# Kernel optimization log

Hardware: AMD Instinct MI355X
Metric: run time of the kernel (lower is better)

The kernel has to match this reference:

```python
import jax, jax.numpy as jnp
import numpy as np

B, LQ, LKV, C, H, Z = 4, 1024, 4096, 256, 8, 1024


def setup_inputs() -> dict:
    key = jax.random.key(0)
    ks = jax.random.split(key, 10)
    s = 0.02  # small init scale for weights
    return {
        "q": jax.random.normal(ks[0], (B, LQ, C), jnp.float32),
        "kv": jax.random.normal(ks[1], (B, LKV, C), jnp.float32),
        "q_ape": jax.random.normal(ks[2], (1, LQ, C), jnp.float32),
        "k_ape": jax.random.normal(ks[3], (1, LKV - Z, C), jnp.float32),
        "attn_pos": jax.random.normal(ks[4], (1, H, LQ, Z), jnp.float32),
        "Wq": jax.random.normal(ks[5], (C, C), jnp.float32) * s,
        "Wk": jax.random.normal(ks[6], (C, C), jnp.float32) * s,
        "Wv": jax.random.normal(ks[7], (C, C), jnp.float32) * s,
        "Wp": jax.random.normal(ks[8], (C, C), jnp.float32) * s,
        "bp": jnp.zeros((C,), jnp.float32),
        "z_shape": Z,
    }


def reference(q, kv, q_ape, k_ape, attn_pos, Wq, Wk, Wv, Wp, bp, z_shape):
    Bn, Lq, Cd = q.shape
    d = Cd // H
    scale = d ** (-0.5)
    # q path: APE added before projection
    qh = ((q + q_ape) @ Wq.T).reshape(Bn, Lq, H, d).transpose(0, 2, 1, 3)  # (B,H,Lq,d)
    # in-place `k[:, z_shape:, :] += k_ape` in torch aliases kv, so v also sees it
    kvm = kv.at[:, z_shape:, :].add(k_ape)
    kh = (kvm @ Wk.T).reshape(Bn, -1, H, d).transpose(0, 2, 1, 3)  # (B,H,Lkv,d)
    vh = (kvm @ Wv.T).reshape(Bn, -1, H, d).transpose(0, 2, 1, 3)  # (B,H,Lkv,d)
    attn = jnp.einsum('bhqd,bhkd->bhqk', qh, kh) * scale           # (B,H,Lq,Lkv)
    # partial positional bias on the template slice only
    attn = attn.at[:, :, :, :z_shape].add(attn_pos)
    attn = jax.nn.softmax(attn, axis=-1)
    x = jnp.einsum('bhqk,bhkd->bhqd', attn, vh)
    x = x.transpose(0, 2, 1, 3).reshape(Bn, Lq, Cd)
    return x @ Wp.T + bp
```

## Files before the change

kernel.cpp:

```cpp
#include <hip/hip_runtime.h>


typedef __attribute__((ext_vector_type(8))) short bf16x8;
typedef __attribute__((ext_vector_type(4))) float f32x4;
typedef __attribute__((ext_vector_type(4))) unsigned short u16x4;

#define MFMA16(a, b, c) __builtin_amdgcn_mfma_f32_16x16x32_bf16((a), (b), (c), 0, 0, 0)

__device__ __forceinline__ unsigned short f2bf(float f) {
  return __builtin_bit_cast(unsigned short, static_cast<__bf16>(f));
}
__device__ __forceinline__ float bf2f(unsigned short u) {
  return __builtin_bit_cast(float, ((unsigned)u) << 16);
}

__global__ __launch_bounds__(256) void prep_all(const float* __restrict__ Wq,
                                                const float* __restrict__ Wk,
                                                const float* __restrict__ Wv,
                                                const float* __restrict__ Wp,
                                                const float* __restrict__ pos,
                                                const float* __restrict__ Xq,
                                                const float* __restrict__ Xkv,
                                                const float* __restrict__ q_ape,
                                                const float* __restrict__ k_ape,
                                                unsigned short* __restrict__ wout,
                                                unsigned short* __restrict__ pfb,
                                                unsigned short* __restrict__ kvp,
                                                unsigned short* __restrict__ qp,
                                                int posBlocks) {
  int bx = blockIdx.x;
  if (bx < posBlocks) {
    const int s4 = bx * 256 + threadIdx.x;
    const int zk4 = s4 & 255, q = (s4 >> 8) & 1023, h = s4 >> 18;
    const float4 v = *(const float4*)(pos + ((size_t)s4 << 2));
    const int kt = zk4 >> 4, c = (zk4 >> 2) & 3, g = zk4 & 3;
    const float L = 1.4426950408889634f;
    u16x4 o = { f2bf(v.x * L), f2bf(v.y * L), f2bf(v.z * L), f2bf(v.w * L) };
    *(u16x4*)(pfb + (size_t)((h << 6) + (q >> 4)) * 16384 + ((kt << 2) + c) * 256 + ((q & 15) << 4) + (g << 2)) = o;
    return;
  }
  bx -= posBlocks;
  if (bx < 128) {
    const int idx = bx * 256 + threadIdx.x;
    const int which = idx >> 13, rem = idx & 8191;
    const int o = rem >> 5, colb = (rem & 31) << 3;
    const float* src = (which == 0) ? Wq : (which == 1) ? Wk : (which == 2) ? Wv : Wp;
    float4 v0 = *(const float4*)(src + (size_t)o * 256 + colb);
    float4 v1 = *(const float4*)(src + (size_t)o * 256 + colb + 4);
    if (which == 0) {
      const float qs = 0.17677669529663687f * 1.4426950408889634f;
      v0.x *= qs; v0.y *= qs; v0.z *= qs; v0.w *= qs;
      v1.x *= qs; v1.y *= qs; v1.z *= qs; v1.w *= qs;
    }
    const int n = o >> 4, x = o & 15, k = colb >> 5, g = (colb & 31) >> 3;
    unsigned short* dst = wout + (which << 16) + n * 4096 + k * 512 + x * 32 + g * 8;
    u16x4 a = { f2bf(v0.x), f2bf(v0.y), f2bf(v0.z), f2bf(v0.w) };
    u16x4 b = { f2bf(v1.x), f2bf(v1.y), f2bf(v1.z), f2bf(v1.w) };
    *(u16x4*)dst = a;
    *(u16x4*)(dst + 4) = b;
    return;
  }
  bx -= 128;
  if (bx < 2048) {
    const int idx = bx * 256 + threadIdx.x;
    const int row = idx >> 5, c8 = idx & 31;
    const int col = c8 << 3, lq = row & 4095;
    const float* xp = Xkv + (size_t)row * 256 + col;
    float4 v0 = *(const float4*)xp, v1 = *(const float4*)(xp + 4);
    if (lq >= 1024) {
      const float* ap = k_ape + (size_t)(lq - 1024) * 256 + col;
      const float4 a0 = *(const float4*)ap, a1 = *(const float4*)(ap + 4);
      v0.x += a0.x; v0.y += a0.y; v0.z += a0.z; v0.w += a0.w;
      v1.x += a1.x; v1.y += a1.y; v1.z += a1.z; v1.w += a1.w;
    }
    const int k = c8 >> 2, g = c8 & 3;
    unsigned short* dst = kvp + (size_t)(row >> 4) * 4096 + k * 512 + (row & 15) * 32 + g * 8;
    u16x4 a = { f2bf(v0.x), f2bf(v0.y), f2bf(v0.z), f2bf(v0.w) };
    u16x4 b = { f2bf(v1.x), f2bf(v1.y), f2bf(v1.z), f2bf(v1.w) };
    *(u16x4*)dst = a;
    *(u16x4*)(dst + 4) = b;
    return;
  }
  bx -= 2048;
  {
    const int idx = bx * 256 + threadIdx.x;
    const int row = idx >> 5, c8 = idx & 31;
    const int col = c8 << 3, arow = row & 1023;
    const float* xp = Xq + (size_t)row * 256 + col;
    const float* ap = q_ape + (size_t)arow * 256 + col;
    const float4 v0 = *(const float4*)xp, v1 = *(const float4*)(xp + 4);
    const float4 a0 = *(const float4*)ap, a1 = *(const float4*)(ap + 4);
    const int k = c8 >> 2, g = c8 & 3;
    unsigned short* dst = qp + (size_t)(row >> 4) * 4096 + k * 512 + (row & 15) * 32 + g * 8;
    u16x4 a = { f2bf(v0.x + a0.x), f2bf(v0.y + a0.y), f2bf(v0.z + a0.z), f2bf(v0.w + a0.w) };
    u16x4 b = { f2bf(v1.x + a1.x), f2bf(v1.y + a1.y), f2bf(v1.z + a1.z), f2bf(v1.w + a1.w) };
    *(u16x4*)dst = a;
    *(u16x4*)(dst + 4) = b;
  }
}

__global__ __launch_bounds__(256, 4) void proj_qkv(const unsigned short* __restrict__ kvp,
                                                   const unsigned short* __restrict__ qp,
                                                   const unsigned short* __restrict__ Wqb,
                                                   const unsigned short* __restrict__ Wkb,
                                                   const unsigned short* __restrict__ Wvb,
                                                   unsigned short* __restrict__ Qhp,
                                                   unsigned short* __restrict__ Khp,
                                                   unsigned short* __restrict__ Vsp) {
  const int tid = threadIdx.x;
  const int w = tid >> 6, lane = tid & 63, x = lane & 15, g = lane >> 4;
  const int rg = w & 1, nh = w >> 1;
  const int bx = blockIdx.x;
  if (bx < 1024) {
    const bool isV = bx >= 512;
    const int bk = isV ? bx - 512 : bx;
    const int rbase = bk * 32 + rg * 16;
    const unsigned short* ap = kvp + (size_t)(rbase >> 4) * 4096 + x * 32 + g * 8;
    bf16x8 a[8];
#pragma unroll
    for (int k = 0; k < 8; ++k) a[k] = *(const bf16x8*)(ap + k * 512);
    const unsigned short* Wb = isV ? Wvb : Wkb;
    f32x4 acc[8];
#pragma unroll
    for (int n = 0; n < 8; ++n) acc[n] = (f32x4){0.f, 0.f, 0.f, 0.f};
#pragma unroll
    for (int k = 0; k < 8; ++k)
#pragma unroll
      for (int n0 = 0; n0 < 8; ++n0) {
        const bf16x8 bw = *(const bf16x8*)(Wb + (size_t)(nh * 8 + n0) * 4096 + k * 512 + x * 32 + g * 8);
        acc[n0] = MFMA16(a[k], bw, acc[n0]);
      }
    if (!isV) {
      const int b2 = rbase >> 12, kk0 = (rbase & 4095) + g * 4;
#pragma unroll
      for (int n0 = 0; n0 < 8; ++n0) {
        const int n = nh * 8 + n0, hh = n >> 1, dd = ((n & 1) << 4) + x;
        unsigned short* kp = Khp + (size_t)(b2 * 8 + hh) * 131072;
#pragma unroll
        for (int r = 0; r < 4; ++r)
          kp[(size_t)(kk0 + r) * 32 + dd] = f2bf(acc[n0][r]);
      }
    } else {
      const int b2 = rbase >> 12, T = (rbase >> 6) & 63, c0 = (rbase >> 4) & 3;
      const int ks = c0 & 1, ih = (c0 >> 1) << 2;
#pragma unroll
      for (int n0 = 0; n0 < 8; ++n0) {
        const int n = nh * 8 + n0, hh = n >> 1, dh = n & 1;
        u16x4 o = { f2bf(acc[n0][0]), f2bf(acc[n0][1]), f2bf(acc[n0][2]), f2bf(acc[n0][3]) };
        *(u16x4*)(Vsp + (size_t)(b2 * 8 + hh) * 131072 + T * 2048 + ks * 1024 + dh * 512 + g * 128 + x * 8 + ih) = o;
      }
    }
  } else {
    const int bq = bx - 1024;
    const int rbase = bq * 32 + rg * 16;
    const unsigned short* ap = qp + (size_t)(rbase >> 4) * 4096 + x * 32 + g * 8;
    bf16x8 a[8];
#pragma unroll
    for (int k = 0; k < 8; ++k) a[k] = *(const bf16x8*)(ap + k * 512);
    f32x4 acc[8];
#pragma unroll
    for (int n = 0; n < 8; ++n) acc[n] = (f32x4){0.f, 0.f, 0.f, 0.f};
#pragma unroll
    for (int k = 0; k < 8; ++k)
#pragma unroll
      for (int n0 = 0; n0 < 8; ++n0) {
        const bf16x8 bw = *(const bf16x8*)(Wqb + (size_t)(nh * 8 + n0) * 4096 + k * 512 + x * 32 + g * 8);
        acc[n0] = MFMA16(a[k], bw, acc[n0]);
      }
    const int b2 = rbase >> 10, qr0 = (rbase & 1023) + g * 4;
#pragma unroll
    for (int n0 = 0; n0 < 8; ++n0) {
      const int n = nh * 8 + n0, hh = n >> 1, dd = ((n & 1) << 4) + x;
      unsigned short* qpn = Qhp + (size_t)(b2 * 8 + hh) * 32768;
#pragma unroll
      for (int r = 0; r < 4; ++r)
        qpn[(size_t)(qr0 + r) * 32 + dd] = f2bf(acc[n0][r]);
    }
  }
}

template <int SPLIT, bool PF>
__global__ __launch_bounds__(256, 4) void
attn_fused(const unsigned short* __restrict__ Qhp,
           const unsigned short* __restrict__ Khp,
           const unsigned short* __restrict__ Vsp,
           const void* __restrict__ pos,
           unsigned short* __restrict__ Xo,
           float* __restrict__ Opart,
           float* __restrict__ lpart) {
  const int tid = threadIdx.x;
  const int w = tid >> 6, lane = tid & 63, x = lane & 15, g = lane >> 4;
  const int bid = blockIdx.x;
  const int h = bid & 7, b = (bid >> 3) & 3, qt = (bid >> 5) & 7, z = bid >> 8;
  const int qrow0 = qt * 128 + w * 32;
  const int NT = 64 / SPLIT;

  const unsigned short* Qpl = Qhp + (size_t)(b * 8 + h) * 32768;
  const bf16x8 aq0 = *(const bf16x8*)(Qpl + (size_t)(qrow0 + x) * 32 + g * 8);
  const bf16x8 aq1 = *(const bf16x8*)(Qpl + (size_t)(qrow0 + 16 + x) * 32 + g * 8);
  const unsigned short* Kpl = Khp + (size_t)(b * 8 + h) * 131072 + x * 32 + g * 8;
  const unsigned short* Vpl = Vsp + (size_t)(b * 8 + h) * 131072 + g * 128 + x * 8;
  const unsigned short* pq0 = PF ? (const unsigned short*)pos + (size_t)((h << 6) + (qt << 3) + (w << 1)) * 16384 : nullptr;
  const unsigned short* pq1 = PF ? pq0 + 16384 : nullptr;
  const float* pr0 = PF ? nullptr : (const float*)pos + (size_t)((h << 10) + qrow0 + x) * 1024;
  const float* pr1 = PF ? nullptr : (const float*)pos + (size_t)((h << 10) + qrow0 + 16 + x) * 1024;
  const f32x4 zc = {0.f, 0.f, 0.f, 0.f};

  f32x4 o00 = zc, o01 = zc, o10 = zc, o11 = zc;
  float ls0 = 0.f, ls1 = 0.f;

  bf16x8 ka[4], va[4];
#pragma unroll
  for (int c = 0; c < 4; ++c)
    ka[c] = *(const bf16x8*)(Kpl + (size_t)((z << 6) + c * 16) * 32);
#pragma unroll
  for (int j = 0; j < 4; ++j)
    va[j] = *(const bf16x8*)(Vpl + (z << 11) + (j << 9));

#define GROUP(AQ, PQ, PR, LS, OA, OB, T, BIAS)                                               \
  do {                                                                                       \
    f32x4 s[4];                                                                              \
    _Pragma("unroll")                                                                        \
    for (int c = 0; c < 4; ++c) s[c] = MFMA16(ka[c], AQ, zc);                                \
    if (BIAS) {                                                                              \
      if (PF) {                                                                              \
        _Pragma("unroll")                                                                    \
        for (int c = 0; c < 4; ++c) {                                                        \
          const u16x4 p = *(const u16x4*)(PQ + ((T) << 10) + (c << 8) + (x << 4) + (g << 2)); \
          s[c][0] += bf2f(p[0]); s[c][1] += bf2f(p[1]);                                      \
          s[c][2] += bf2f(p[2]); s[c][3] += bf2f(p[3]);                                      \
        }                                                                                    \
      } else {                                                                               \
        const float LOG2E = 1.4426950408889634f;                                             \
        _Pragma("unroll")                                                                    \
        for (int c = 0; c < 4; ++c) {                                                        \
          const float4 p = *(const float4*)(PR + ((T) << 6) + c * 16 + g * 4);               \
          s[c][0] = fmaf(p.x, LOG2E, s[c][0]); s[c][1] = fmaf(p.y, LOG2E, s[c][1]);          \
          s[c][2] = fmaf(p.z, LOG2E, s[c][2]); s[c][3] = fmaf(p.w, LOG2E, s[c][3]);          \
        }                                                                                    \
      }                                                                                      \
    }                                                                                        \
    _Pragma("unroll")                                                                        \
    for (int c = 0; c < 4; ++c)                                                              \
      _Pragma("unroll")                                                                      \
      for (int r = 0; r < 4; ++r) {                                                          \
        s[c][r] = __builtin_amdgcn_exp2f(s[c][r]); LS += s[c][r];                            \
      }                                                                                      \
    bf16x8 pa0, pa1;                                                                         \
    _Pragma("unroll")                                                                        \
    for (int r = 0; r < 4; ++r) {                                                            \
      pa0[r] = (short)f2bf(s[0][r]); pa0[4 + r] = (short)f2bf(s[2][r]);                      \
      pa1[r] = (short)f2bf(s[1][r]); pa1[4 + r] = (short)f2bf(s[3][r]);                      \
    }                                                                                        \
    OA = MFMA16(pa0, va[0], OA); OB = MFMA16(pa0, va[1], OB);                                \
    OA = MFMA16(pa1, va[2], OA); OB = MFMA16(pa1, va[3], OB);                                \
  } while (0)

#define TILE(T, BIAS)                                                                        \
  do {                                                                                       \
    const int tp = ((T) + SPLIT <= 63) ? (T) + SPLIT : (T);                                  \
    GROUP(aq0, pq0, pr0, ls0, o00, o01, T, BIAS);                                            \
    GROUP(aq1, pq1, pr1, ls1, o10, o11, T, BIAS);                                            \
    _Pragma("unroll")                                                                        \
    for (int c = 0; c < 4; ++c)                            \
      ka[c] = *(const bf16x8*)(Kpl + (size_t)((tp << 6) + c * 16) * 32);                     \
    _Pragma("unroll")                                                                        \
    for (int j = 0; j < 4; ++j)                            \
      va[j] = *(const bf16x8*)(Vpl + (tp << 11) + (j << 9));                                 \
  } while (0)

  const int nb = 16 / SPLIT;
  int t = z;
  for (int i = 0; i < nb; ++i) { TILE(t, true);  t += SPLIT; }
  for (int i = nb; i < NT; ++i) { TILE(t, false); t += SPLIT; }
#undef TILE
#undef GROUP

  ls0 += __shfl_xor(ls0, 16); ls0 += __shfl_xor(ls0, 32);
  ls1 += __shfl_xor(ls1, 16); ls1 += __shfl_xor(ls1, 32);

  if (SPLIT == 1) {
    const float inv0 = 1.f / ls0, inv1 = 1.f / ls1;
#pragma unroll
    for (int r = 0; r < 4; ++r) {
      const float ir0 = __shfl(inv0, g * 4 + r, 64);
      const float ir1 = __shfl(inv1, g * 4 + r, 64);
      const size_t orow0 = (size_t)((b << 10) + qrow0 + g * 4 + r) * 256 + h * 32;
      const size_t orow1 = (size_t)((b << 10) + qrow0 + 16 + g * 4 + r) * 256 + h * 32;
      Xo[orow0 + x] = f2bf(o00[r] * ir0);
      Xo[orow0 + 16 + x] = f2bf(o01[r] * ir0);
      Xo[orow1 + x] = f2bf(o10[r] * ir1);
      Xo[orow1 + 16 + x] = f2bf(o11[r] * ir1);
    }
  } else {
    if (g == 0) {
      lpart[(size_t)z * 32768 + ((b << 10) + qrow0 + x) * 8 + h] = ls0;
      lpart[(size_t)z * 32768 + ((b << 10) + qrow0 + 16 + x) * 8 + h] = ls1;
    }
#pragma unroll
    for (int r = 0; r < 4; ++r) {
      const size_t orow0 = (size_t)z * 1048576 + (size_t)((b << 10) + qrow0 + g * 4 + r) * 256 + h * 32;
      const size_t orow1 = (size_t)z * 1048576 + (size_t)((b << 10) + qrow0 + 16 + g * 4 + r) * 256 + h * 32;
      Opart[orow0 + x] = o00[r];
      Opart[orow0 + 16 + x] = o01[r];
      Opart[orow1 + x] = o10[r];
      Opart[orow1 + 16 + x] = o11[r];
    }
  }
}

__global__ __launch_bounds__(256) void combine(const float* __restrict__ Opart,
                                               const float* __restrict__ lpart,
                                               unsigned short* __restrict__ Xo, int split) {
  const int idx = blockIdx.x * 256 + threadIdx.x;
  const int row = idx >> 6, c4 = (idx & 63) << 2, h = c4 >> 5;
  float l = 0.f;
  float4 o = {0.f, 0.f, 0.f, 0.f};
  for (int zz = 0; zz < split; ++zz) {
    l += lpart[(size_t)zz * 32768 + row * 8 + h];
    const float4 ov = *(const float4*)(Opart + (size_t)zz * 1048576 + (size_t)row * 256 + c4);
    o.x += ov.x; o.y += ov.y; o.z += ov.z; o.w += ov.w;
  }
  const float inv = 1.f / l;
  u16x4 pk = { f2bf(o.x * inv), f2bf(o.y * inv), f2bf(o.z * inv), f2bf(o.w * inv) };
  *(u16x4*)(Xo + (size_t)row * 256 + c4) = pk;
}

__global__ __launch_bounds__(256) void proj_out(const unsigned short* __restrict__ Xb,
                                                const unsigned short* __restrict__ Wb,
                                                const float* __restrict__ bias,
                                                float* __restrict__ out) {
  const int tid = threadIdx.x;
  const int w = tid >> 6, lane = tid & 63, x = lane & 15, g = lane >> 4;
  const int rbase = blockIdx.x << 4;
  const int cb = w << 6;
  bf16x8 a[8];
#pragma unroll
  for (int k = 0; k < 8; ++k)
    a[k] = *(const bf16x8*)(Xb + (size_t)(rbase + x) * 256 + k * 32 + g * 8);
  f32x4 acc[4];
#pragma unroll
  for (int n = 0; n < 4; ++n) acc[n] = (f32x4){0.f, 0.f, 0.f, 0.f};
#pragma unroll
  for (int k = 0; k < 8; ++k)
#pragma unroll
    for (int n = 0; n < 4; ++n) {
      const bf16x8 bw = *(const bf16x8*)(Wb + (size_t)((w << 2) + n) * 4096 + k * 512 + x * 32 + g * 8);
      acc[n] = MFMA16(a[k], bw, acc[n]);
    }
#pragma unroll
  for (int n = 0; n < 4; ++n) {
    const float bv = bias[cb + n * 16 + x];
#pragma unroll
    for (int r = 0; r < 4; ++r)
      out[(size_t)(rbase + g * 4 + r) * 256 + cb + n * 16 + x] = acc[n][r] + bv;
  }
}

extern "C" void kernel_launch(void* const* d_in, const int* in_sizes, int n_in,
                              void* d_out, int out_size, void* d_ws, size_t ws_size,
                              hipStream_t stream) {
  const float* q        = (const float*)d_in[0];
  const float* kv       = (const float*)d_in[1];
  const float* q_ape    = (const float*)d_in[2];
  const float* k_ape    = (const float*)d_in[3];
  const float* attn_pos = (const float*)d_in[4];
  const float* Wq       = (const float*)d_in[5];
  const float* Wk       = (const float*)d_in[6];
  const float* Wv       = (const float*)d_in[7];
  const float* Wp       = (const float*)d_in[8];
  const float* bp       = (const float*)d_in[9];
  float* out = (float*)d_out;

  unsigned short* wsb = (unsigned short*)d_ws;
  unsigned short* Wqb = wsb;
  unsigned short* Wkb = wsb + 65536;
  unsigned short* Wvb = wsb + 131072;
  unsigned short* Wpb = wsb + 196608;
  unsigned short* Qhp = wsb + 262144;
  unsigned short* Khp = wsb + 1310720;
  unsigned short* Vsp = wsb + 5505024;
  unsigned short* Xws = wsb + 9699328;
  unsigned short* kvp = wsb + 10747904;
  unsigned short* qp  = wsb + 14942208;

  const size_t L0  = 31981568ull;
  const size_t PFB = 16777216ull;
  const size_t PS  = 4325376ull;
  int split; bool havepf;
  if      (ws_size >= L0 + PFB + 4 * PS) { split = 4; havepf = true; }
  else if (ws_size >= L0 + 4 * PS)       { split = 4; havepf = false; }
  else if (ws_size >= L0 + 2 * PS)       { split = 2; havepf = false; }
  else                                   { split = 1; havepf = false; }
  unsigned short* pfb = (unsigned short*)((char*)d_ws + L0);
  float* Opart = (float*)((char*)d_ws + L0 + (havepf ? PFB : 0));
  float* lpart = Opart + (size_t)split * 1048576;

  const int posBlocks = havepf ? 8192 : 0;
  prep_all<<<posBlocks + 128 + 2048 + 512, 256, 0, stream>>>(
      Wq, Wk, Wv, Wp, attn_pos, q, kv, q_ape, k_ape, wsb, pfb, kvp, qp, posBlocks);
  proj_qkv<<<1152, 256, 0, stream>>>(kvp, qp, Wqb, Wkb, Wvb, Qhp, Khp, Vsp);
  if (havepf)
    attn_fused<4, true><<<1024, 256, 0, stream>>>(Qhp, Khp, Vsp, pfb, Xws, Opart, lpart);
  else if (split == 4)
    attn_fused<4, false><<<1024, 256, 0, stream>>>(Qhp, Khp, Vsp, attn_pos, Xws, Opart, lpart);
  else if (split == 2)
    attn_fused<2, false><<<512, 256, 0, stream>>>(Qhp, Khp, Vsp, attn_pos, Xws, Opart, lpart);
  else
    attn_fused<1, false><<<256, 256, 0, stream>>>(Qhp, Khp, Vsp, attn_pos, Xws, Opart, lpart);
  if (split > 1) combine<<<1024, 256, 0, stream>>>(Opart, lpart, Xws, split);
  proj_out<<<256, 256, 0, stream>>>(Xws, Wpb, bp, out);
}
```

Baseline: 88.84 us.

## Process 64 query rows per wave, raise KV split to 8, pre-tile attention output

Each wave now handles four 16-row query groups instead of two, so every K/V fragment loaded from global memory is reused across twice as many query rows. To keep the grid size, the KV dimension is split eight ways when workspace allows. The combine and single-split paths now write the attention output in an MFMA-fragment tiled layout, which proj_out reads contiguously. The cost is more accumulator registers per wave, which may lower occupancy under the 4-blocks launch bound, plus more partial outputs for combine to read and sum.

```diff
diff --git a/kernel.cpp b/kernel.cpp
--- a/kernel.cpp
+++ b/kernel.cpp
@@ -191,23 +191,25 @@
   const int tid = threadIdx.x;
   const int w = tid >> 6, lane = tid & 63, x = lane & 15, g = lane >> 4;
   const int bid = blockIdx.x;
-  const int h = bid & 7, b = (bid >> 3) & 3, qt = (bid >> 5) & 7, z = bid >> 8;
-  const int qrow0 = qt * 128 + w * 32;
+  const int h = bid & 7, b = (bid >> 3) & 3, qt = (bid >> 5) & 3, z = bid >> 7;
+  const int qrow0 = qt * 256 + w * 64;
   const int NT = 64 / SPLIT;
 
   const unsigned short* Qpl = Qhp + (size_t)(b * 8 + h) * 32768;
-  const bf16x8 aq0 = *(const bf16x8*)(Qpl + (size_t)(qrow0 + x) * 32 + g * 8);
-  const bf16x8 aq1 = *(const bf16x8*)(Qpl + (size_t)(qrow0 + 16 + x) * 32 + g * 8);
+  bf16x8 aq[4];
+#pragma unroll
+  for (int gi = 0; gi < 4; ++gi)
+    aq[gi] = *(const bf16x8*)(Qpl + (size_t)(qrow0 + gi * 16 + x) * 32 + g * 8);
   const unsigned short* Kpl = Khp + (size_t)(b * 8 + h) * 131072 + x * 32 + g * 8;
   const unsigned short* Vpl = Vsp + (size_t)(b * 8 + h) * 131072 + g * 128 + x * 8;
-  const unsigned short* pq0 = PF ? (const unsigned short*)pos + (size_t)((h << 6) + (qt << 3) + (w << 1)) * 16384 : nullptr;
-  const unsigned short* pq1 = PF ? pq0 + 16384 : nullptr;
-  const float* pr0 = PF ? nullptr : (const float*)pos + (size_t)((h << 10) + qrow0 + x) * 1024;
-  const float* pr1 = PF ? nullptr : (const float*)pos + (size_t)((h << 10) + qrow0 + 16 + x) * 1024;
+  const unsigned short* pqb = PF ? (const unsigned short*)pos + (size_t)((h << 6) + (qt << 4) + (w << 2)) * 16384 : nullptr;
+  const float* prb = PF ? nullptr : (const float*)pos + (size_t)((h << 10) + qrow0 + x) * 1024;
   const f32x4 zc = {0.f, 0.f, 0.f, 0.f};
 
-  f32x4 o00 = zc, o01 = zc, o10 = zc, o11 = zc;
-  float ls0 = 0.f, ls1 = 0.f;
+  f32x4 oA[4], oB[4];
+  float ls[4];
+#pragma unroll
+  for (int gi = 0; gi < 4; ++gi) { oA[gi] = zc; oB[gi] = zc; ls[gi] = 0.f; }
 
   bf16x8 ka[4], va[4];
 #pragma unroll
@@ -217,50 +219,53 @@
   for (int j = 0; j < 4; ++j)
     va[j] = *(const bf16x8*)(Vpl + (z << 11) + (j << 9));
 
-#define GROUP(AQ, PQ, PR, LS, OA, OB, T, BIAS)                                               \
+#define CPAIR(GI, C0, C1, V0, V1, T, BIAS)                                                   \
   do {                                                                                       \
-    f32x4 s[4];                                                                              \
-    _Pragma("unroll")                                                                        \
-    for (int c = 0; c < 4; ++c) s[c] = MFMA16(ka[c], AQ, zc);                                \
+    f32x4 s0 = MFMA16(ka[C0], aq[GI], zc);                                                   \
+    f32x4 s1 = MFMA16(ka[C1], aq[GI], zc);                                                   \
     if (BIAS) {                                                                              \
       if (PF) {                                                                              \
-        _Pragma("unroll")                                                                    \
-        for (int c = 0; c < 4; ++c) {                                                        \
-          const u16x4 p = *(const u16x4*)(PQ + ((T) << 10) + (c << 8) + (x << 4) + (g << 2)); \
-          s[c][0] += bf2f(p[0]); s[c][1] += bf2f(p[1]);                                      \
-          s[c][2] += bf2f(p[2]); s[c][3] += bf2f(p[3]);                                      \
-        }                                                                                    \
+        const unsigned short* pq = pqb + (size_t)(GI) * 16384;                               \
+        const u16x4 p0 = *(const u16x4*)(pq + ((T) << 10) + ((C0) << 8) + (x << 4) + (g << 2)); \
+        const u16x4 p1 = *(const u16x4*)(pq + ((T) << 10) + ((C1) << 8) + (x << 4) + (g << 2)); \
+        s0[0] += bf2f(p0[0]); s0[1] += bf2f(p0[1]); s0[2] += bf2f(p0[2]); s0[3] += bf2f(p0[3]); \
+        s1[0] += bf2f(p1[0]); s1[1] += bf2f(p1[1]); s1[2] += bf2f(p1[2]); s1[3] += bf2f(p1[3]); \
       } else {                                                                               \
         const float LOG2E = 1.4426950408889634f;                                             \
-        _Pragma("unroll")                                                                    \
-        for (int c = 0; c < 4; ++c) {                                                        \
-          const float4 p = *(const float4*)(PR + ((T) << 6) + c * 16 + g * 4);               \
-          s[c][0] = fmaf(p.x, LOG2E, s[c][0]); s[c][1] = fmaf(p.y, LOG2E, s[c][1]);          \
-          s[c][2] = fmaf(p.z, LOG2E, s[c][2]); s[c][3] = fmaf(p.w, LOG2E, s[c][3]);          \
-        }                                                                                    \
+        const float* pr = prb + (size_t)(GI) * 16384;                                        \
+        const float4 p0 = *(const float4*)(pr + ((T) << 6) + (C0) * 16 + g * 4);             \
+        const float4 p1 = *(const float4*)(pr + ((T) << 6) + (C1) * 16 + g * 4);             \
+        s0[0] = fmaf(p0.x, LOG2E, s0[0]); s0[1] = fmaf(p0.y, LOG2E, s0[1]);                  \
+        s0[2] = fmaf(p0.z, LOG2E, s0[2]); s0[3] = fmaf(p0.w, LOG2E, s0[3]);                  \
+        s1[0] = fmaf(p1.x, LOG2E, s1[0]); s1[1] = fmaf(p1.y, LOG2E, s1[1]);                  \
+        s1[2] = fmaf(p1.z, LOG2E, s1[2]); s1[3] = fmaf(p1.w, LOG2E, s1[3]);                  \
       }                                                                                      \
     }                                                                                        \
-    _Pragma("unroll")                                                                        \
-    for (int c = 0; c < 4; ++c)                                                              \
-      _Pragma("unroll")                                                                      \
-      for (int r = 0; r < 4; ++r) {                                                          \
-        s[c][r] = __builtin_amdgcn_exp2f(s[c][r]); LS += s[c][r];                            \
-      }                                                                                      \
-    bf16x8 pa0, pa1;                                                                         \
+    bf16x8 pa;                                                                               \
     _Pragma("unroll")                                                                        \
     for (int r = 0; r < 4; ++r) {                                                            \
-      pa0[r] = (short)f2bf(s[0][r]); pa0[4 + r] = (short)f2bf(s[2][r]);                      \
-      pa1[r] = (short)f2bf(s[1][r]); pa1[4 + r] = (short)f2bf(s[3][r]);                      \
+      s0[r] = __builtin_amdgcn_exp2f(s0[r]); ls[GI] += s0[r];                                \
+      s1[r] = __builtin_amdgcn_exp2f(s1[r]); ls[GI] += s1[r];                                \
+      pa[r] = (short)f2bf(s0[r]);                                                            \
+      pa[4 + r] = (short)f2bf(s1[r]);                                                        \
     }                                                                                        \
-    OA = MFMA16(pa0, va[0], OA); OB = MFMA16(pa0, va[1], OB);                                \
-    OA = MFMA16(pa1, va[2], OA); OB = MFMA16(pa1, va[3], OB);                                \
+    oA[GI] = MFMA16(pa, va[V0], oA[GI]);                                                     \
+    oB[GI] = MFMA16(pa, va[V1], oB[GI]);                                                     \
+  } while (0)
+
+#define GROUP(GI, T, BIAS)                                                                   \
+  do {                                                                                       \
+    CPAIR(GI, 0, 2, 0, 1, T, BIAS);                                                          \
+    CPAIR(GI, 1, 3, 2, 3, T, BIAS);                                                          \
   } while (0)
 
 #define TILE(T, BIAS)                                                                        \
   do {                                                                                       \
     const int tp = ((T) + SPLIT <= 63) ? (T) + SPLIT : (T);                                  \
-    GROUP(aq0, pq0, pr0, ls0, o00, o01, T, BIAS);                                            \
-    GROUP(aq1, pq1, pr1, ls1, o10, o11, T, BIAS);                                            \
+    GROUP(0, T, BIAS);                                                                       \
+    GROUP(1, T, BIAS);                                                                       \
+    GROUP(2, T, BIAS);                                                                       \
+    GROUP(3, T, BIAS);                                                                       \
     _Pragma("unroll")                                                                        \
     for (int c = 0; c < 4; ++c)                            \
       ka[c] = *(const bf16x8*)(Kpl + (size_t)((tp << 6) + c * 16) * 32);                     \
@@ -275,36 +280,39 @@
   for (int i = nb; i < NT; ++i) { TILE(t, false); t += SPLIT; }
 #undef TILE
 #undef GROUP
-
-  ls0 += __shfl_xor(ls0, 16); ls0 += __shfl_xor(ls0, 32);
-  ls1 += __shfl_xor(ls1, 16); ls1 += __shfl_xor(ls1, 32);
+#undef CPAIR
+
+#pragma unroll
+  for (int gi = 0; gi < 4; ++gi) {
+    ls[gi] += __shfl_xor(ls[gi], 16);
+    ls[gi] += __shfl_xor(ls[gi], 32);
+  }
 
   if (SPLIT == 1) {
-    const float inv0 = 1.f / ls0, inv1 = 1.f / ls1;
-#pragma unroll
-    for (int r = 0; r < 4; ++r) {
-      const float ir0 = __shfl(inv0, g * 4 + r, 64);
-      const float ir1 = __shfl(inv1, g * 4 + r, 64);
-      const size_t orow0 = (size_t)((b << 10) + qrow0 + g * 4 + r) * 256 + h * 32;
-      const size_t orow1 = (size_t)((b << 10) + qrow0 + 16 + g * 4 + r) * 256 + h * 32;
-      Xo[orow0 + x] = f2bf(o00[r] * ir0);
-      Xo[orow0 + 16 + x] = f2bf(o01[r] * ir0);
-      Xo[orow1 + x] = f2bf(o10[r] * ir1);
-      Xo[orow1 + 16 + x] = f2bf(o11[r] * ir1);
+#pragma unroll
+    for (int gi = 0; gi < 4; ++gi) {
+      const float inv = 1.f / ls[gi];
+      const int rowblk = (b << 6) + (qt << 4) + (w << 2) + gi;
+#pragma unroll
+      for (int r = 0; r < 4; ++r) {
+        const float ir = __shfl(inv, g * 4 + r, 64);
+        unsigned short* dst = Xo + (size_t)rowblk * 4096 + h * 512 + (g * 4 + r) * 32;
+        dst[x] = f2bf(oA[gi][r] * ir);
+        dst[16 + x] = f2bf(oB[gi][r] * ir);
+      }
     }
   } else {
-    if (g == 0) {
-      lpart[(size_t)z * 32768 + ((b << 10) + qrow0 + x) * 8 + h] = ls0;
-      lpart[(size_t)z * 32768 + ((b << 10) + qrow0 + 16 + x) * 8 + h] = ls1;
-    }
-#pragma unroll
-    for (int r = 0; r < 4; ++r) {
-      const size_t orow0 = (size_t)z * 1048576 + (size_t)((b << 10) + qrow0 + g * 4 + r) * 256 + h * 32;
-      const size_t orow1 = (size_t)z * 1048576 + (size_t)((b << 10) + qrow0 + 16 + g * 4 + r) * 256 + h * 32;
-      Opart[orow0 + x] = o00[r];
-      Opart[orow0 + 16 + x] = o01[r];
-      Opart[orow1 + x] = o10[r];
-      Opart[orow1 + 16 + x] = o11[r];
+#pragma unroll
+    for (int gi = 0; gi < 4; ++gi) {
+      if (g == 0)
+        lpart[(size_t)z * 32768 + ((b << 10) + qrow0 + gi * 16 + x) * 8 + h] = ls[gi];
+#pragma unroll
+      for (int r = 0; r < 4; ++r) {
+        const size_t orow = (size_t)z * 1048576 +
+            (size_t)((b << 10) + qrow0 + gi * 16 + g * 4 + r) * 256 + h * 32;
+        Opart[orow + x] = oA[gi][r];
+        Opart[orow + 16 + x] = oB[gi][r];
+      }
     }
   }
 }
@@ -323,10 +331,12 @@
   }
   const float inv = 1.f / l;
   u16x4 pk = { f2bf(o.x * inv), f2bf(o.y * inv), f2bf(o.z * inv), f2bf(o.w * inv) };
-  *(u16x4*)(Xo + (size_t)row * 256 + c4) = pk;
-}
-
-__global__ __launch_bounds__(256) void proj_out(const unsigned short* __restrict__ Xb,
+  unsigned short* dst = Xo + (size_t)(row >> 4) * 4096 + h * 512 +
+                        (row & 15) * 32 + ((c4 >> 3) & 3) * 8 + (c4 & 7);
+  *(u16x4*)dst = pk;
+}
+
+__global__ __launch_bounds__(256) void proj_out(const unsigned short* __restrict__ Xp,
                                                 const unsigned short* __restrict__ Wb,
                                                 const float* __restrict__ bias,
                                                 float* __restrict__ out) {
@@ -334,10 +344,10 @@
   const int w = tid >> 6, lane = tid & 63, x = lane & 15, g = lane >> 4;
   const int rbase = blockIdx.x << 4;
   const int cb = w << 6;
+  const unsigned short* ap = Xp + (size_t)blockIdx.x * 4096 + x * 32 + g * 8;
   bf16x8 a[8];
 #pragma unroll
-  for (int k = 0; k < 8; ++k)
-    a[k] = *(const bf16x8*)(Xb + (size_t)(rbase + x) * 256 + k * 32 + g * 8);
+  for (int k = 0; k < 8; ++k) a[k] = *(const bf16x8*)(ap + k * 512);
   f32x4 acc[4];
 #pragma unroll
   for (int n = 0; n < 4; ++n) acc[n] = (f32x4){0.f, 0.f, 0.f, 0.f};
@@ -388,7 +398,8 @@
   const size_t PFB = 16777216ull;
   const size_t PS  = 4325376ull;
   int split; bool havepf;
-  if      (ws_size >= L0 + PFB + 4 * PS) { split = 4; havepf = true; }
+  if      (ws_size >= L0 + PFB + 8 * PS) { split = 8; havepf = true; }
+  else if (ws_size >= L0 + PFB + 4 * PS) { split = 4; havepf = true; }
   else if (ws_size >= L0 + 4 * PS)       { split = 4; havepf = false; }
   else if (ws_size >= L0 + 2 * PS)       { split = 2; havepf = false; }
   else                                   { split = 1; havepf = false; }
@@ -400,14 +411,16 @@
   prep_all<<<posBlocks + 128 + 2048 + 512, 256, 0, stream>>>(
       Wq, Wk, Wv, Wp, attn_pos, q, kv, q_ape, k_ape, wsb, pfb, kvp, qp, posBlocks);
   proj_qkv<<<1152, 256, 0, stream>>>(kvp, qp, Wqb, Wkb, Wvb, Qhp, Khp, Vsp);
-  if (havepf)
-    attn_fused<4, true><<<1024, 256, 0, stream>>>(Qhp, Khp, Vsp, pfb, Xws, Opart, lpart);
+  if (havepf && split == 8)
+    attn_fused<8, true><<<1024, 256, 0, stream>>>(Qhp, Khp, Vsp, pfb, Xws, Opart, lpart);
+  else if (havepf)
+    attn_fused<4, true><<<512, 256, 0, stream>>>(Qhp, Khp, Vsp, pfb, Xws, Opart, lpart);
   else if (split == 4)
-    attn_fused<4, false><<<1024, 256, 0, stream>>>(Qhp, Khp, Vsp, attn_pos, Xws, Opart, lpart);
+    attn_fused<4, false><<<512, 256, 0, stream>>>(Qhp, Khp, Vsp, attn_pos, Xws, Opart, lpart);
   else if (split == 2)
-    attn_fused<2, false><<<512, 256, 0, stream>>>(Qhp, Khp, Vsp, attn_pos, Xws, Opart, lpart);
+    attn_fused<2, false><<<256, 256, 0, stream>>>(Qhp, Khp, Vsp, attn_pos, Xws, Opart, lpart);
   else
-    attn_fused<1, false><<<256, 256, 0, stream>>>(Qhp, Khp, Vsp, attn_pos, Xws, Opart, lpart);
+    attn_fused<1, false><<<128, 256, 0, stream>>>(Qhp, Khp, Vsp, attn_pos, Xws, Opart, lpart);
   if (split > 1) combine<<<1024, 256, 0, stream>>>(Opart, lpart, Xws, split);
   proj_out<<<256, 256, 0, stream>>>(Xws, Wpb, bp, out);
 }
```

New measurement: 96.51 us. +8.6%, slower.
